# Kernel tuning notes

Hardware: AMD Instinct MI355X
Metric: run time of the kernel (lower is better)

The kernel has to match this reference:

```python
import jax, jax.numpy as jnp
import numpy as np

EPS = 1e-5


def bn(x, g, b, m, v):
    # eval-mode BatchNorm2d: x [B,C,H,W], params [C]
    s = g / jnp.sqrt(v + EPS)
    return x * s[None, :, None, None] + (b - m * s)[None, :, None, None]


def conv1x1(x, w):
    # x [B,C,H,W], w [O,C]
    return jnp.einsum('bchw,oc->bohw', x, w)


def offset_conv(x, w, b):
    # 3x3 conv, stride 1, pad 1, with bias; x [B,C,H,W], w [18,C,3,3]
    y = jax.lax.conv_general_dilated(x, w, window_strides=(1, 1),
                                     padding=((1, 1), (1, 1)),
                                     dimension_numbers=('NCHW', 'OIHW', 'NCHW'))
    return y + b[None, :, None, None]


def deform_conv3x3(x, offset, w):
    # DeformConv v1: x [B,C,H,W], offset [B,18,H,W] ((dy,dx) pairs per kernel
    # point, torchvision layout), w [O,C,3,3]; stride=1, pad=1, dil=1.
    B, C, H, W = x.shape
    oy = offset[:, 0::2]  # [B,9,H,W]
    ox = offset[:, 1::2]  # [B,9,H,W]
    kgy = (jnp.arange(9) // 3 - 1).astype(x.dtype)  # kernel y offsets
    kgx = (jnp.arange(9) % 3 - 1).astype(x.dtype)   # kernel x offsets
    hh = jnp.arange(H, dtype=x.dtype)
    ww = jnp.arange(W, dtype=x.dtype)
    py = hh[None, None, :, None] + kgy[None, :, None, None] + oy  # [B,9,H,W]
    px = ww[None, None, None, :] + kgx[None, :, None, None] + ox  # [B,9,H,W]
    feat = jnp.transpose(x, (0, 2, 3, 1))  # [B,H,W,C]
    y0 = jnp.floor(py)
    x0 = jnp.floor(px)
    wy = py - y0
    wx = px - x0
    bidx = jnp.arange(B).reshape(B, 1, 1, 1)
    acc = jnp.zeros((B, 9, H, W, C), dtype=x.dtype)
    for dy in (0, 1):
        for dx in (0, 1):
            yi = y0 + dy
            xi = x0 + dx
            wgt = (wy if dy else 1.0 - wy) * (wx if dx else 1.0 - wx)
            valid = (yi >= 0) & (yi <= H - 1) & (xi >= 0) & (xi <= W - 1)
            yic = jnp.clip(yi, 0, H - 1).astype(jnp.int32)
            xic = jnp.clip(xi, 0, W - 1).astype(jnp.int32)
            g = feat[bidx, yic, xic]  # gather -> [B,9,H,W,C]
            acc = acc + (wgt * valid.astype(x.dtype))[..., None] * g
    wk = w.reshape(w.shape[0], C, 9)  # k = ky*3+kx matches kgy/kgx order
    return jnp.einsum('bkhwc,ock->bohw', acc, wk)


def setup_inputs() -> dict:
    key = jax.random.key(0)
    ks = jax.random.split(key, 20)
    B, Cin, H, W = 16, 1024, 32, 32
    P, O = 256, 1024  # width / outplanes
    f32 = jnp.float32
    d = {}
    d['x'] = jax.random.normal(ks[0], (B, Cin, H, W), f32)
    d['w1'] = jax.random.normal(ks[1], (P, Cin), f32) * 0.02
    d['bn1_g'] = 1.0 + 0.1 * jax.random.normal(ks[2], (P,), f32)
    d['bn1_b'] = 0.1 * jax.random.normal(ks[3], (P,), f32)
    d['bn1_m'] = 0.1 * jax.random.normal(ks[4], (P,), f32)
    d['bn1_v'] = 0.5 + jax.random.uniform(ks[5], (P,), f32)
    d['off_w'] = jax.random.normal(ks[6], (18, P, 3, 3), f32) * 0.01
    d['off_b'] = 0.01 * jax.random.normal(ks[7], (18,), f32)
    d['w2'] = jax.random.normal(ks[8], (P, P, 3, 3), f32) * 0.02
    d['bn2_g'] = 1.0 + 0.1 * jax.random.normal(ks[9], (P,), f32)
    d['bn2_b'] = 0.1 * jax.random.normal(ks[10], (P,), f32)
    d['bn2_m'] = 0.1 * jax.random.normal(ks[11], (P,), f32)
    d['bn2_v'] = 0.5 + jax.random.uniform(ks[12], (P,), f32)
    d['w3'] = jax.random.normal(ks[13], (O, P), f32) * 0.02
    d['bn3_g'] = 1.0 + 0.1 * jax.random.normal(ks[14], (O,), f32)
    d['bn3_b'] = 0.1 * jax.random.normal(ks[15], (O,), f32)
    d['bn3_m'] = 0.1 * jax.random.normal(ks[16], (O,), f32)
    d['bn3_v'] = 0.5 + jax.random.uniform(ks[17], (O,), f32)
    return d


def reference(x, w1, bn1_g, bn1_b, bn1_m, bn1_v, off_w, off_b, w2,
              bn2_g, bn2_b, bn2_m, bn2_v, w3, bn3_g, bn3_b, bn3_m, bn3_v):
    shortcut = x
    h = jax.nn.relu(bn(conv1x1(x, w1), bn1_g, bn1_b, bn1_m, bn1_v))
    offset = offset_conv(h, off_w, off_b)
    h = deform_conv3x3(h, offset, w2)
    h = jax.nn.relu(bn(h, bn2_g, bn2_b, bn2_m, bn2_v))
    h = bn(conv1x1(h, w3), bn3_g, bn3_b, bn3_m, bn3_v)
    return jax.nn.relu(h + shortcut)
```

## Files before the change

kernel.cpp:

```cpp
#include <hip/hip_runtime.h>

#define BN_EPS 1e-5f

typedef __bf16 bf16_t;
typedef __bf16 bf16x8 __attribute__((ext_vector_type(8)));
typedef float f32x4 __attribute__((ext_vector_type(4)));


__global__ void __launch_bounds__(1024) k_bnprep(
    const float* g1, const float* b1, const float* m1, const float* v1,
    const float* g2, const float* b2, const float* m2, const float* v2,
    const float* g3, const float* b3, const float* m3, const float* v3,
    float* bnc) {
    int t = threadIdx.x;
    if (t < 256) {
        float s = g1[t] * rsqrtf(v1[t] + BN_EPS);
        bnc[t] = s;
        bnc[256 + t] = b1[t] - m1[t] * s;
        float s2 = g2[t] * rsqrtf(v2[t] + BN_EPS);
        bnc[512 + t] = s2;
        bnc[768 + t] = b2[t] - m2[t] * s2;
    }
    float s3 = g3[t] * rsqrtf(v3[t] + BN_EPS);
    bnc[1024 + t] = s3;
    bnc[2048 + t] = b3[t] - m3[t] * s3;
}

__global__ void __launch_bounds__(256) k_cast(const float* __restrict__ s,
                                              bf16_t* __restrict__ d, int n4) {
    int i = blockIdx.x * 256 + threadIdx.x;
    if (i >= n4) return;
    float4 v = ((const float4*)s)[i];
    d[4 * i + 0] = (bf16_t)v.x;
    d[4 * i + 1] = (bf16_t)v.y;
    d[4 * i + 2] = (bf16_t)v.z;
    d[4 * i + 3] = (bf16_t)v.w;
}

__global__ void __launch_bounds__(256) k_w2f(const float* __restrict__ w2,
                                             bf16_t* __restrict__ w2f) {
    int idx = blockIdx.x * 256 + threadIdx.x;
    if (idx >= 73728) return;
    int lane = idx & 63;
    int rest = idx >> 6;
    int nt = rest & 15;
    int rest2 = rest >> 4;
    int p = rest2 & 7;
    int kp = rest2 >> 3;
    int n = nt * 16 + (lane & 15);
    int c0 = p * 32 + (lane >> 4) * 8;
    bf16x8 r;
#pragma unroll
    for (int e = 0; e < 8; ++e)
        r[e] = (bf16_t)w2[(size_t)n * 2304 + (c0 + e) * 9 + kp];
    *(bf16x8*)(w2f + (size_t)idx * 8) = r;
}

__global__ void __launch_bounds__(256) k_owtb(const float* __restrict__ ow,
                                              bf16_t* __restrict__ owtb) {
    int idx = blockIdx.x * 256 + threadIdx.x;
    if (idx >= 73728) return;
    int j = idx / 2304;
    int rem = idx - j * 2304;
    int kp = rem >> 8;
    int c = rem & 255;
    float v = (j < 18) ? ow[(j * 256 + c) * 9 + kp] : 0.f;
    owtb[idx] = (bf16_t)v;
}

__global__ void __launch_bounds__(256) k_xb(const float* __restrict__ x,
                                            bf16_t* __restrict__ xb) {
    __shared__ float ld[64 * 68];
    int t = threadIdx.x;
    int hw0 = blockIdx.x * 64, c0 = blockIdx.y * 64, b = blockIdx.z;
    int ci = t >> 2, h0 = (t & 3) * 16;
    const float* src = x + ((size_t)(b * 1024 + c0 + ci) << 10) + hw0 + h0;
#pragma unroll
    for (int i = 0; i < 4; ++i)
        *(float4*)(ld + ci * 68 + h0 + 4 * i) = *(const float4*)(src + 4 * i);
    __syncthreads();
    int r = t >> 2, cc0 = (t & 3) * 16;
    bf16x8 o0, o1;
#pragma unroll
    for (int i = 0; i < 8; ++i) o0[i] = (bf16_t)ld[(cc0 + i) * 68 + r];
#pragma unroll
    for (int i = 0; i < 8; ++i) o1[i] = (bf16_t)ld[(cc0 + 8 + i) * 68 + r];
    bf16_t* dst = xb + ((size_t)(b * 1024 + hw0 + r) << 10) + c0 + cc0;
    *(bf16x8*)dst = o0;
    *(bf16x8*)(dst + 8) = o1;
}

__global__ void __launch_bounds__(256) k_gemm64(
    const bf16_t* __restrict__ A, const bf16_t* __restrict__ Bt, int K, int ldo,
    const float* __restrict__ sc, const float* __restrict__ sh,
    const float* __restrict__ resid, bf16_t* __restrict__ outb,
    float* __restrict__ outf, int epi) {
    __shared__ __align__(16) bf16_t As[64 * 40];
    __shared__ __align__(16) bf16_t Bs[128 * 40];
    int t = threadIdx.x;
    int lane = t & 63;
    int w = t >> 6;
    int wm = w >> 1, wn = w & 1;
    int m0 = blockIdx.x * 64, n0 = blockIdx.y * 128;

    int ar = t >> 2, as_ = t & 3;
    const bf16_t* ag = A + (size_t)(m0 + ar) * K + as_ * 8;
    int aw = ar * 40 + ((as_ ^ (ar & 3)) * 8);
    int bn0 = t >> 2, bs_ = t & 3;
    const bf16_t* bg0 = Bt + (size_t)(n0 + bn0) * K + bs_ * 8;
    const bf16_t* bg1 = Bt + (size_t)(n0 + 64 + bn0) * K + bs_ * 8;
    int bw0 = bn0 * 40 + ((bs_ ^ (bn0 & 3)) * 8);
    int bw1 = (64 + bn0) * 40 + ((bs_ ^ (bn0 & 3)) * 8);

    int asel = lane >> 4;
    int ar0 = wm * 32 + (lane & 15);
    int aoff0 = ar0 * 40 + ((asel ^ (ar0 & 3)) * 8);
    int aoff1 = (ar0 + 16) * 40 + ((asel ^ (ar0 & 3)) * 8);
    int boff[4];
#pragma unroll
    for (int ni = 0; ni < 4; ++ni) {
        int n = wn * 64 + ni * 16 + (lane & 15);
        boff[ni] = n * 40 + ((asel ^ (n & 3)) * 8);
    }
    f32x4 acc[2][4] = {};

    for (int k0 = 0; k0 < K; k0 += 32) {
        __syncthreads();
        *(bf16x8*)(As + aw) = *(const bf16x8*)(ag + k0);
        *(bf16x8*)(Bs + bw0) = *(const bf16x8*)(bg0 + k0);
        *(bf16x8*)(Bs + bw1) = *(const bf16x8*)(bg1 + k0);
        __syncthreads();
        bf16x8 a0 = *(const bf16x8*)(As + aoff0);
        bf16x8 a1 = *(const bf16x8*)(As + aoff1);
#pragma unroll
        for (int ni = 0; ni < 4; ++ni) {
            bf16x8 bv = *(const bf16x8*)(Bs + boff[ni]);
            acc[0][ni] = __builtin_amdgcn_mfma_f32_16x16x32_bf16(a0, bv, acc[0][ni], 0, 0, 0);
            acc[1][ni] = __builtin_amdgcn_mfma_f32_16x16x32_bf16(a1, bv, acc[1][ni], 0, 0, 0);
        }
    }

    int mrb = m0 + wm * 32 + (lane >> 4) * 4;
    int ncb = n0 + wn * 64 + (lane & 15);
    if (epi == 0) {
#pragma unroll
        for (int mi = 0; mi < 2; ++mi)
#pragma unroll
            for (int ni = 0; ni < 4; ++ni) {
                int n = ncb + ni * 16;
                float s = sc[n], h = sh[n];
#pragma unroll
                for (int j = 0; j < 4; ++j) {
                    int m = mrb + mi * 16 + j;
                    float v = fmaxf(fmaf(acc[mi][ni][j], s, h), 0.f);
                    outb[(size_t)m * ldo + n] = (bf16_t)v;
                }
            }
    } else {
#pragma unroll
        for (int mi = 0; mi < 2; ++mi) {
            int m = mrb + mi * 16;
            int bb = m >> 10, hw = m & 1023;
#pragma unroll
            for (int ni = 0; ni < 4; ++ni) {
                int o = ncb + ni * 16;
                float s = sc[o], h = sh[o];
                size_t idx = (((size_t)(bb * 1024 + o)) << 10) + hw;
                float4 r = *(const float4*)(resid + idx);
                float4 v;
                v.x = fmaxf(fmaf(acc[mi][ni][0], s, h) + r.x, 0.f);
                v.y = fmaxf(fmaf(acc[mi][ni][1], s, h) + r.y, 0.f);
                v.z = fmaxf(fmaf(acc[mi][ni][2], s, h) + r.z, 0.f);
                v.w = fmaxf(fmaf(acc[mi][ni][3], s, h) + r.w, 0.f);
                *(float4*)(outf + idx) = v;
            }
        }
    }
}

__global__ void __launch_bounds__(256) k_off(const bf16_t* __restrict__ h1,
                                             const bf16_t* __restrict__ owtb,
                                             const float* __restrict__ offb,
                                             float* __restrict__ off) {
    int t = threadIdx.x;
    int lane = t & 63;
    int w = t >> 6;
    int mi = w >> 1, ni = w & 1;
    int y = blockIdx.x, b = blockIdx.y;
    int x = (lane & 15) + mi * 16;
    int ksel = lane >> 4;
    int j = (lane & 15) + ni * 16;
    f32x4 acc = {};
    const bf16_t* h1base = h1 + ((size_t)b << 18);
    const bf16_t* brow = owtb + (size_t)j * 2304 + ksel * 8;

    for (int kp = 0; kp < 9; ++kp) {
        int yy = y + kp / 3 - 1;
        int xx = x + kp % 3 - 1;
        bool vy = (yy >= 0) && (yy < 32);
        bool vx = (xx >= 0) && (xx < 32);
        const bf16_t* arow = h1base + (((size_t)(yy * 32 + xx)) << 8) + ksel * 8;
        const bf16_t* bp = brow + kp * 256;
#pragma unroll
        for (int s = 0; s < 8; ++s) {
            bf16x8 av = {};
            if (vy && vx) av = *(const bf16x8*)(arow + s * 32);
            bf16x8 bv = *(const bf16x8*)(bp + s * 32);
            acc = __builtin_amdgcn_mfma_f32_16x16x32_bf16(av, bv, acc, 0, 0, 0);
        }
    }
    if (j < 18) {
        float bias = offb[j];
        size_t ob = (size_t)b * 18432 + (size_t)j * 1024 + y * 32 + mi * 16;
#pragma unroll
        for (int r = 0; r < 4; ++r) {
            off[ob + ksel * 4 + r] = acc[r] + bias;
        }
    }
}

__global__ void __launch_bounds__(256) k_deform(const bf16_t* __restrict__ h1,
                                                const float* __restrict__ off,
                                                const bf16_t* __restrict__ w2f,
                                                const float* __restrict__ bnc,
                                                bf16_t* __restrict__ h2) {
    __shared__ __align__(16) bf16_t As[8 * 1288];
    int t = threadIdx.x;
    int lane = t & 63;
    int wn = t >> 6;
    int y = blockIdx.x, b = blockIdx.y;
    int sx = t >> 3, scg = t & 7;
    int asel = lane >> 4;
    int ar0 = lane & 15;
    int aoff0 = ar0 * 40 + ((asel ^ (ar0 & 3)) * 8);
    int aoff1 = (ar0 + 16) * 40 + ((asel ^ ((ar0 + 16) & 3)) * 8);
    const bf16_t* wfl = w2f + (size_t)(wn * 256 + lane) * 8;
    f32x4 acc[2][4] = {};
    size_t obase = (size_t)b * 18432 + (size_t)y * 32 + sx;
    size_t h1row = (size_t)b * 1024;

    for (int k = 0; k < 9; ++k) {
        __syncthreads();
        float oy = off[obase + (size_t)(2 * k) * 1024];
        float ox = off[obase + (size_t)(2 * k + 1) * 1024];
        float py = (float)y + (float)(k / 3 - 1) + oy;
        float px = (float)sx + (float)(k % 3 - 1) + ox;
        float fy = floorf(py), fx = floorf(px);
        float wy = py - fy, wx = px - fx;
        int y0 = (int)fy, x0 = (int)fx;
        int y1 = y0 + 1, x1 = x0 + 1;
        float vy0 = (y0 >= 0 && y0 < 32) ? 1.f : 0.f;
        float vy1 = (y1 >= 0 && y1 < 32) ? 1.f : 0.f;
        float vx0 = (x0 >= 0 && x0 < 32) ? 1.f : 0.f;
        float vx1 = (x1 >= 0 && x1 < 32) ? 1.f : 0.f;
        int yc0 = min(max(y0, 0), 31), yc1 = min(max(y1, 0), 31);
        int xc0 = min(max(x0, 0), 31), xc1 = min(max(x1, 0), 31);
        float w00 = (1.f - wy) * (1.f - wx) * vy0 * vx0;
        float w01 = (1.f - wy) * wx * vy0 * vx1;
        float w10 = wy * (1.f - wx) * vy1 * vx0;
        float w11 = wy * wx * vy1 * vx1;
        const bf16_t* p00 = h1 + ((h1row + yc0 * 32 + xc0) << 8);
        const bf16_t* p01 = h1 + ((h1row + yc0 * 32 + xc1) << 8);
        const bf16_t* p10 = h1 + ((h1row + yc1 * 32 + xc0) << 8);
        const bf16_t* p11 = h1 + ((h1row + yc1 * 32 + xc1) << 8);
        bf16_t* pnl = As + scg * 1288 + sx * 40;
#pragma unroll
        for (int q = 0; q < 4; ++q) {
            int c = scg * 32 + q * 8;
            bf16x8 v00 = *(const bf16x8*)(p00 + c);
            bf16x8 v01 = *(const bf16x8*)(p01 + c);
            bf16x8 v10 = *(const bf16x8*)(p10 + c);
            bf16x8 v11 = *(const bf16x8*)(p11 + c);
            bf16x8 r;
#pragma unroll
            for (int e = 0; e < 8; ++e) {
                float f = w00 * (float)v00[e] + w01 * (float)v01[e] +
                          w10 * (float)v10[e] + w11 * (float)v11[e];
                r[e] = (bf16_t)f;
            }
            *(bf16x8*)(pnl + ((q ^ (sx & 3)) * 8)) = r;
        }
        __syncthreads();
#pragma unroll
        for (int p = 0; p < 8; ++p) {
            const bf16_t* pb = As + p * 1288;
            bf16x8 a0 = *(const bf16x8*)(pb + aoff0);
            bf16x8 a1 = *(const bf16x8*)(pb + aoff1);
            const bf16_t* wf = wfl + (size_t)(k * 8 + p) * 8192;
#pragma unroll
            for (int ni = 0; ni < 4; ++ni) {
                bf16x8 bv = *(const bf16x8*)(wf + ni * 512);
                acc[0][ni] = __builtin_amdgcn_mfma_f32_16x16x32_bf16(a0, bv, acc[0][ni], 0, 0, 0);
                acc[1][ni] = __builtin_amdgcn_mfma_f32_16x16x32_bf16(a1, bv, acc[1][ni], 0, 0, 0);
            }
        }
    }
    int mrb = (lane >> 4) * 4;
    int ncb = wn * 64 + (lane & 15);
#pragma unroll
    for (int mi = 0; mi < 2; ++mi)
#pragma unroll
        for (int ni = 0; ni < 4; ++ni) {
            int n = ncb + ni * 16;
            float s = bnc[512 + n], h = bnc[768 + n];
#pragma unroll
            for (int j = 0; j < 4; ++j) {
                int row = mrb + mi * 16 + j;
                float v = fmaxf(fmaf(acc[mi][ni][j], s, h), 0.f);
                h2[(((size_t)(b * 1024 + y * 32 + row)) << 8) + n] = (bf16_t)v;
            }
        }
}

extern "C" void kernel_launch(void* const* d_in, const int* in_sizes, int n_in,
                              void* d_out, int out_size, void* d_ws, size_t ws_size,
                              hipStream_t stream) {
    const float* x = (const float*)d_in[0];
    const float* w1 = (const float*)d_in[1];
    const float* bn1g = (const float*)d_in[2];
    const float* bn1b = (const float*)d_in[3];
    const float* bn1m = (const float*)d_in[4];
    const float* bn1v = (const float*)d_in[5];
    const float* off_w = (const float*)d_in[6];
    const float* off_b = (const float*)d_in[7];
    const float* w2 = (const float*)d_in[8];
    const float* bn2g = (const float*)d_in[9];
    const float* bn2b = (const float*)d_in[10];
    const float* bn2m = (const float*)d_in[11];
    const float* bn2v = (const float*)d_in[12];
    const float* w3 = (const float*)d_in[13];
    const float* bn3g = (const float*)d_in[14];
    const float* bn3b = (const float*)d_in[15];
    const float* bn3m = (const float*)d_in[16];
    const float* bn3v = (const float*)d_in[17];
    float* out = (float*)d_out;

    char* ws = (char*)d_ws;
    float* bnc = (float*)(ws + 0);
    bf16_t* owtb = (bf16_t*)(ws + 12288);
    float* off = (float*)(ws + 178176);
    bf16_t* xb = (bf16_t*)(ws + 1357824);
    bf16_t* w1b = (bf16_t*)(ws + 34912256);
    bf16_t* w2fb = (bf16_t*)(ws + 35436544);
    bf16_t* w3b = (bf16_t*)(ws + 36616192);
    bf16_t* h1b = (bf16_t*)(ws + 37140480);
    bf16_t* h2b = (bf16_t*)(ws + 45529088);

    k_bnprep<<<1, 1024, 0, stream>>>(bn1g, bn1b, bn1m, bn1v, bn2g, bn2b, bn2m,
                                     bn2v, bn3g, bn3b, bn3m, bn3v, bnc);
    k_cast<<<256, 256, 0, stream>>>(w1, w1b, 65536);
    k_cast<<<256, 256, 0, stream>>>(w3, w3b, 65536);
    k_w2f<<<288, 256, 0, stream>>>(w2, w2fb);
    k_owtb<<<288, 256, 0, stream>>>(off_w, owtb);
    k_xb<<<dim3(16, 16, 16), 256, 0, stream>>>(x, xb);
    k_gemm64<<<dim3(256, 2), 256, 0, stream>>>(xb, w1b, 1024, 256, bnc,
                                               bnc + 256, nullptr, h1b, nullptr, 0);
    k_off<<<dim3(32, 16), 256, 0, stream>>>(h1b, owtb, off_b, off);
    k_deform<<<dim3(32, 16), 256, 0, stream>>>(h1b, off, w2fb, bnc, h2b);
    k_gemm64<<<dim3(256, 8), 256, 0, stream>>>(h2b, w3b, 256, 1024, bnc + 1024,
                                               bnc + 2048, x, nullptr, out, 1);
}
```

Measured before the change: 358.4 us.

## Double-buffer deform-conv gather tile and prefetch weight fragments ahead of MFMA

The deform conv kernel now keeps two LDS buffers for the bilinear-sampled tile. It issues the global gathers for kernel point k+1 before running the MFMAs for point k, and writes the converted tile into the other buffer halfway through the MFMA loop. Weight fragments are also prefetched two slices ahead into registers. This hides the gather and weight-load latency behind matrix math and drops one barrier per iteration. In exchange it doubles LDS use and holds more live registers (four sets of gathered vectors plus weight buffers), which can lower occupancy.

```diff
diff --git a/kernel.cpp b/kernel.cpp
--- a/kernel.cpp
+++ b/kernel.cpp
@@ -224,7 +224,7 @@
                                                 const bf16_t* __restrict__ w2f,
                                                 const float* __restrict__ bnc,
                                                 bf16_t* __restrict__ h2) {
-    __shared__ __align__(16) bf16_t As[8 * 1288];
+    __shared__ __align__(16) bf16_t As[2][8 * 1288];
     int t = threadIdx.x;
     int lane = t & 63;
     int wn = t >> 6;
@@ -239,8 +239,10 @@
     size_t obase = (size_t)b * 18432 + (size_t)y * 32 + sx;
     size_t h1row = (size_t)b * 1024;
 
-    for (int k = 0; k < 9; ++k) {
-        __syncthreads();
+    bf16x8 g00[4], g01[4], g10[4], g11[4];
+    float w00, w01, w10, w11;
+
+    auto issue_gather = [&](int k) {
         float oy = off[obase + (size_t)(2 * k) * 1024];
         float ox = off[obase + (size_t)(2 * k + 1) * 1024];
         float py = (float)y + (float)(k / 3 - 1) + oy;
@@ -255,45 +257,87 @@
         float vx1 = (x1 >= 0 && x1 < 32) ? 1.f : 0.f;
         int yc0 = min(max(y0, 0), 31), yc1 = min(max(y1, 0), 31);
         int xc0 = min(max(x0, 0), 31), xc1 = min(max(x1, 0), 31);
-        float w00 = (1.f - wy) * (1.f - wx) * vy0 * vx0;
-        float w01 = (1.f - wy) * wx * vy0 * vx1;
-        float w10 = wy * (1.f - wx) * vy1 * vx0;
-        float w11 = wy * wx * vy1 * vx1;
+        w00 = (1.f - wy) * (1.f - wx) * vy0 * vx0;
+        w01 = (1.f - wy) * wx * vy0 * vx1;
+        w10 = wy * (1.f - wx) * vy1 * vx0;
+        w11 = wy * wx * vy1 * vx1;
         const bf16_t* p00 = h1 + ((h1row + yc0 * 32 + xc0) << 8);
         const bf16_t* p01 = h1 + ((h1row + yc0 * 32 + xc1) << 8);
         const bf16_t* p10 = h1 + ((h1row + yc1 * 32 + xc0) << 8);
         const bf16_t* p11 = h1 + ((h1row + yc1 * 32 + xc1) << 8);
-        bf16_t* pnl = As + scg * 1288 + sx * 40;
 #pragma unroll
         for (int q = 0; q < 4; ++q) {
             int c = scg * 32 + q * 8;
-            bf16x8 v00 = *(const bf16x8*)(p00 + c);
-            bf16x8 v01 = *(const bf16x8*)(p01 + c);
-            bf16x8 v10 = *(const bf16x8*)(p10 + c);
-            bf16x8 v11 = *(const bf16x8*)(p11 + c);
+            g00[q] = *(const bf16x8*)(p00 + c);
+            g01[q] = *(const bf16x8*)(p01 + c);
+            g10[q] = *(const bf16x8*)(p10 + c);
+            g11[q] = *(const bf16x8*)(p11 + c);
+        }
+    };
+    auto cvt_write = [&](int buf) {
+        bf16_t* pnl = &As[buf][scg * 1288 + sx * 40];
+#pragma unroll
+        for (int q = 0; q < 4; ++q) {
             bf16x8 r;
 #pragma unroll
             for (int e = 0; e < 8; ++e) {
-                float f = w00 * (float)v00[e] + w01 * (float)v01[e] +
-                          w10 * (float)v10[e] + w11 * (float)v11[e];
+                float f = w00 * (float)g00[q][e] + w01 * (float)g01[q][e] +
+                          w10 * (float)g10[q][e] + w11 * (float)g11[q][e];
                 r[e] = (bf16_t)f;
             }
             *(bf16x8*)(pnl + ((q ^ (sx & 3)) * 8)) = r;
         }
-        __syncthreads();
-#pragma unroll
-        for (int p = 0; p < 8; ++p) {
-            const bf16_t* pb = As + p * 1288;
+    };
+
+    issue_gather(0);
+    cvt_write(0);
+    __syncthreads();
+
+    for (int k = 0; k < 9; ++k) {
+        int cur = k & 1;
+        if (k < 8) issue_gather(k + 1);
+        const bf16_t* wfk = wfl + (size_t)k * 65536;
+        bf16x8 bb[2][4];
+#pragma unroll
+        for (int ni = 0; ni < 4; ++ni)
+            bb[0][ni] = *(const bf16x8*)(wfk + ni * 512);
+#pragma unroll
+        for (int ni = 0; ni < 4; ++ni)
+            bb[1][ni] = *(const bf16x8*)(wfk + 8192 + ni * 512);
+#pragma unroll
+        for (int p = 0; p < 4; ++p) {
+            const bf16_t* pb = &As[cur][p * 1288];
             bf16x8 a0 = *(const bf16x8*)(pb + aoff0);
             bf16x8 a1 = *(const bf16x8*)(pb + aoff1);
-            const bf16_t* wf = wfl + (size_t)(k * 8 + p) * 8192;
 #pragma unroll
             for (int ni = 0; ni < 4; ++ni) {
-                bf16x8 bv = *(const bf16x8*)(wf + ni * 512);
+                bf16x8 bv = bb[p & 1][ni];
                 acc[0][ni] = __builtin_amdgcn_mfma_f32_16x16x32_bf16(a0, bv, acc[0][ni], 0, 0, 0);
                 acc[1][ni] = __builtin_amdgcn_mfma_f32_16x16x32_bf16(a1, bv, acc[1][ni], 0, 0, 0);
             }
-        }
+#pragma unroll
+            for (int ni = 0; ni < 4; ++ni)
+                bb[p & 1][ni] = *(const bf16x8*)(wfk + (p + 2) * 8192 + ni * 512);
+        }
+        if (k < 8) cvt_write(cur ^ 1);
+#pragma unroll
+        for (int p = 4; p < 8; ++p) {
+            const bf16_t* pb = &As[cur][p * 1288];
+            bf16x8 a0 = *(const bf16x8*)(pb + aoff0);
+            bf16x8 a1 = *(const bf16x8*)(pb + aoff1);
+#pragma unroll
+            for (int ni = 0; ni < 4; ++ni) {
+                bf16x8 bv = bb[p & 1][ni];
+                acc[0][ni] = __builtin_amdgcn_mfma_f32_16x16x32_bf16(a0, bv, acc[0][ni], 0, 0, 0);
+                acc[1][ni] = __builtin_amdgcn_mfma_f32_16x16x32_bf16(a1, bv, acc[1][ni], 0, 0, 0);
+            }
+            if (p + 2 < 8) {
+#pragma unroll
+                for (int ni = 0; ni < 4; ++ni)
+                    bb[p & 1][ni] = *(const bf16x8*)(wfk + (p + 2) * 8192 + ni * 512);
+            }
+        }
+        __syncthreads();
     }
     int mrb = (lane >> 4) * 4;
     int ncb = wn * 64 + (lane & 15);
```

New measurement: 294.3 us. 17.9% less time.
